# Kernel optimization log

Measured on AMD Instinct MI355X. Metric: run time of the kernel, lower is better.

## Reference

```python
import jax, jax.numpy as jnp
import numpy as np

TEXT_SIZE = 1024
HIDDEN = 512

def setup_inputs() -> dict:
    key = jax.random.key(0)
    k1, k2, k3, k4, k5, k6 = jax.random.split(key, 6)
    B, S, D, H = 32, 4096, TEXT_SIZE, HIDDEN
    text_seq = jax.random.normal(k1, (B, S, D), dtype=jnp.float32)
    previous_hidden = jax.random.normal(k2, (B, D), dtype=jnp.float32)
    # attention_hidden: Linear(D -> H) + ReLU
    W1 = jax.random.normal(k3, (D, H), dtype=jnp.float32) / np.sqrt(D)
    b1 = jax.random.normal(k4, (H,), dtype=jnp.float32) * 0.01
    # attention_scoring: Linear(H -> 1)
    w2 = jax.random.normal(k5, (H,), dtype=jnp.float32) / np.sqrt(H)
    b2 = jax.random.normal(k6, (), dtype=jnp.float32) * 0.01
    return {"text_seq": text_seq, "previous_hidden": previous_hidden,
            "W1": W1, "b1": b1, "w2": w2, "b2": b2}

def reference(text_seq, previous_hidden, W1, b1, w2, b2):
    # text_seq: [B, S, D]; previous_hidden: [B, D]
    # per-timestep: score = Linear1(ReLU(Linear0(prev * h_t))) -> batched here
    prod = text_seq * previous_hidden[:, None, :]          # [B, S, D]
    hidden = jax.nn.relu(jnp.einsum('bsd,dh->bsh', prod, W1) + b1)  # [B, S, H]
    scores = jnp.einsum('bsh,h->bs', hidden, w2) + b2      # [B, S]
    weights = jax.nn.softmax(scores, axis=1)               # [B, S]
    out = jnp.einsum('bsd,bs->bd', text_seq, weights)      # [B, D]
    return out
```

## Files before the change

kernel.cpp:

```cpp
#include <hip/hip_runtime.h>
#include <hip/hip_bf16.h>
#include <stdint.h>

#define B_ 32
#define S_ 4096
#define D_ 1024
#define H_ 512
#define BK 32

typedef __bf16 bf16_t;
typedef bf16_t bf16x8 __attribute__((ext_vector_type(8)));
typedef float f32x4 __attribute__((ext_vector_type(4)));

#define AS_STRIDE 40

__global__ __launch_bounds__(256)
void ta_prep_kernel(const float* __restrict__ W1, bf16_t* __restrict__ W1bf)
{
    const int kb = blockIdx.x;
    const int t  = threadIdx.x;

#pragma unroll
    for (int hh = 0; hh < 2; ++hh) {
        int h = t + hh * 256;
        bf16_t row[BK];
#pragma unroll
        for (int kk = 0; kk < BK; ++kk)
            row[kk] = (bf16_t)W1[(size_t)(kb * BK + kk) * H_ + h];
        bf16_t* dst = W1bf + ((size_t)kb * H_ + h) * BK;
#pragma unroll
        for (int c = 0; c < 4; ++c)
            *(bf16x8*)(dst + c * 8) = *(const bf16x8*)&row[c * 8];
    }
}

__global__ __launch_bounds__(256, 2)
void ta_score_kernel(const float* __restrict__ x,
                     const float* __restrict__ prev,
                     const bf16_t* __restrict__ W1bf,
                     const float* __restrict__ b1,
                     const float* __restrict__ w2,
                     const float* __restrict__ b2,
                     float* __restrict__ scores)
{
    __shared__ bf16_t As[64 * AS_STRIDE];
    __shared__ bf16_t Bs[H_ * BK];
    __shared__ float  scoreS[4][64];

    const int t    = threadIdx.x;
    const int wv   = t >> 6;
    const int lane = t & 63;
    const int quad = lane >> 4;
    const int n16  = lane & 15;

    const int b  = blockIdx.y;
    const int s0 = blockIdx.x * 64;

    const int ar = t >> 2;
    const int ac = (t & 3) * 8;
    const float* xrow  = x + ((size_t)b * S_ + s0 + ar) * D_;
    const float* prevb = prev + (size_t)b * D_;

    float b1v[8], w2v[8];
#pragma unroll
    for (int j = 0; j < 8; ++j) {
        int h = wv * 128 + j * 16 + n16;
        b1v[j] = b1[h];
        w2v[j] = w2[h];
    }

    f32x4 acc[4][8];
#pragma unroll
    for (int i = 0; i < 4; ++i)
#pragma unroll
        for (int j = 0; j < 8; ++j)
            acc[i][j] = (f32x4){0.f, 0.f, 0.f, 0.f};

    for (int kb = 0; kb < D_ / BK; ++kb) {
        f32x4 a0 = *(const f32x4*)(xrow + kb * BK + ac);
        f32x4 a1 = *(const f32x4*)(xrow + kb * BK + ac + 4);
        f32x4 p0 = *(const f32x4*)(prevb + kb * BK + ac);
        f32x4 p1 = *(const f32x4*)(prevb + kb * BK + ac + 4);

        __syncthreads();

        const char* gB = (const char*)(W1bf + (size_t)kb * H_ * BK);
#pragma unroll
        for (int r = 0; r < 8; ++r) {
            int off = (wv * 8 + r) * 1024;
            __builtin_amdgcn_global_load_lds(
                (const __attribute__((address_space(1))) void*)(gB + off + lane * 16),
                (__attribute__((address_space(3))) void*)((char*)Bs + off),
                16, 0, 0);
        }

        {
            a0 *= p0;
            a1 *= p1;
            bf16x8 aw;
#pragma unroll
            for (int e = 0; e < 4; ++e) { aw[e] = (bf16_t)a0[e]; aw[4 + e] = (bf16_t)a1[e]; }
            *(bf16x8*)&As[ar * AS_STRIDE + ac] = aw;
        }

        __syncthreads();

        bf16x8 afr[4];
#pragma unroll
        for (int i = 0; i < 4; ++i)
            afr[i] = *(const bf16x8*)&As[(i * 16 + n16) * AS_STRIDE + quad * 8];
#pragma unroll
        for (int j = 0; j < 8; ++j) {
            bf16x8 bfr = *(const bf16x8*)&Bs[(wv * 128 + j * 16 + n16) * BK + quad * 8];
#pragma unroll
            for (int i = 0; i < 4; ++i)
                acc[i][j] = __builtin_amdgcn_mfma_f32_16x16x32_bf16(afr[i], bfr, acc[i][j], 0, 0, 0);
        }
    }

    float part[4][4];
#pragma unroll
    for (int i = 0; i < 4; ++i)
#pragma unroll
        for (int r = 0; r < 4; ++r) {
            float p = 0.f;
#pragma unroll
            for (int j = 0; j < 8; ++j) {
                float hval = acc[i][j][r] + b1v[j];
                hval = fmaxf(hval, 0.f);
                p += hval * w2v[j];
            }
            for (int off = 8; off > 0; off >>= 1)
                p += __shfl_xor(p, off);
            part[i][r] = p;
        }

    if (n16 == 0) {
#pragma unroll
        for (int i = 0; i < 4; ++i)
#pragma unroll
            for (int r = 0; r < 4; ++r)
                scoreS[wv][i * 16 + quad * 4 + r] = part[i][r];
    }
    __syncthreads();

    if (t < 64) {
        float sc = scoreS[0][t] + scoreS[1][t] + scoreS[2][t] + scoreS[3][t] + b2[0];
        scores[(size_t)b * S_ + s0 + t] = sc;
    }
}

__global__ __launch_bounds__(256)
void ta_softmax_kernel(const float* __restrict__ scores, float* __restrict__ weights)
{
    const int b = blockIdx.x;
    const int t = threadIdx.x;
    const float* s = scores + (size_t)b * S_;

    float v[16];
    float m = -1e30f;
#pragma unroll
    for (int i = 0; i < 16; ++i) {
        v[i] = s[t + i * 256];
        m = fmaxf(m, v[i]);
    }

    __shared__ float red[256];
    red[t] = m;
    __syncthreads();
    for (int off = 128; off > 0; off >>= 1) {
        if (t < off) red[t] = fmaxf(red[t], red[t + off]);
        __syncthreads();
    }
    m = red[0];
    __syncthreads();

    float sum = 0.f;
#pragma unroll
    for (int i = 0; i < 16; ++i) {
        v[i] = __expf(v[i] - m);
        sum += v[i];
    }
    red[t] = sum;
    __syncthreads();
    for (int off = 128; off > 0; off >>= 1) {
        if (t < off) red[t] += red[t + off];
        __syncthreads();
    }
    const float inv = 1.f / red[0];

    float* w = weights + (size_t)b * S_;
#pragma unroll
    for (int i = 0; i < 16; ++i)
        w[t + i * 256] = v[i] * inv;
}

__global__ __launch_bounds__(256)
void ta_wsum_kernel(const float* __restrict__ x, const float* __restrict__ weights,
                    float* __restrict__ out)
{
    const int sc = blockIdx.x;
    const int b  = blockIdx.y;
    const int t  = threadIdx.x;

    __shared__ float wS[128];
    if (t < 128) wS[t] = weights[(size_t)b * S_ + sc * 128 + t];
    __syncthreads();

    const float* xb = x + ((size_t)b * S_ + (size_t)sc * 128) * D_;

    f32x4 acc0 = (f32x4){0.f,0.f,0.f,0.f}, acc1 = acc0, acc2 = acc0, acc3 = acc0;
    for (int s = 0; s < 128; s += 4) {
        f32x4 x0 = *(const f32x4*)(xb + (size_t)(s + 0) * D_ + t * 4);
        f32x4 x1 = *(const f32x4*)(xb + (size_t)(s + 1) * D_ + t * 4);
        f32x4 x2 = *(const f32x4*)(xb + (size_t)(s + 2) * D_ + t * 4);
        f32x4 x3 = *(const f32x4*)(xb + (size_t)(s + 3) * D_ + t * 4);
        acc0 += x0 * wS[s + 0];
        acc1 += x1 * wS[s + 1];
        acc2 += x2 * wS[s + 2];
        acc3 += x3 * wS[s + 3];
    }
    f32x4 r = (acc0 + acc1) + (acc2 + acc3);

    float* o = out + (size_t)b * D_ + t * 4;
    atomicAdd(o + 0, r[0]);
    atomicAdd(o + 1, r[1]);
    atomicAdd(o + 2, r[2]);
    atomicAdd(o + 3, r[3]);
}

extern "C" void kernel_launch(void* const* d_in, const int* in_sizes, int n_in,
                              void* d_out, int out_size, void* d_ws, size_t ws_size,
                              hipStream_t stream) {
    const float* x    = (const float*)d_in[0];
    const float* prev = (const float*)d_in[1];
    const float* W1   = (const float*)d_in[2];
    const float* b1   = (const float*)d_in[3];
    const float* w2   = (const float*)d_in[4];
    const float* b2   = (const float*)d_in[5];
    float* out = (float*)d_out;

    bf16_t* W1bf   = (bf16_t*)d_ws;
    float* scores  = (float*)((char*)d_ws + (size_t)1024 * 1024);
    float* weights = scores + B_ * S_;

    hipMemsetAsync(d_out, 0, (size_t)B_ * D_ * sizeof(float), stream);

    ta_prep_kernel<<<32, 256, 0, stream>>>(W1, W1bf);

    dim3 g1(S_ / 64, B_);
    ta_score_kernel<<<g1, 256, 0, stream>>>(x, prev, W1bf, b1, w2, b2, scores);

    ta_softmax_kernel<<<B_, 256, 0, stream>>>(scores, weights);

    dim3 g3(S_ / 128, B_);
    ta_wsum_kernel<<<g3, 256, 0, stream>>>(x, weights, out);
}
```

Measured before the change: 875.5 us.

## Fuse score, softmax and weighted sum via flash-style chunked online softmax

Folds the softmax and weighted-sum stages into the score kernel. Each 64-row block computes a local max and exp-sum, forms its partial weighted sum of x while that tile is likely still cached, and writes the partial plus (m, l) to workspace. A small combine kernel rescales and sums the 64 partials per batch. This is meant to avoid a second full pass over x from HBM, two kernel launches, the memset and the atomics, at the cost of an 8 MB partial buffer and an extra combine step.

```diff
diff --git a/kernel.cpp b/kernel.cpp
--- a/kernel.cpp
+++ b/kernel.cpp
@@ -7,6 +7,7 @@
 #define D_ 1024
 #define H_ 512
 #define BK 32
+#define NCHUNK 64
 
 typedef __bf16 bf16_t;
 typedef bf16_t bf16x8 __attribute__((ext_vector_type(8)));
@@ -35,17 +36,19 @@
 }
 
 __global__ __launch_bounds__(256, 2)
-void ta_score_kernel(const float* __restrict__ x,
+void ta_fused_kernel(const float* __restrict__ x,
                      const float* __restrict__ prev,
                      const bf16_t* __restrict__ W1bf,
                      const float* __restrict__ b1,
                      const float* __restrict__ w2,
                      const float* __restrict__ b2,
-                     float* __restrict__ scores)
+                     float* __restrict__ pout,
+                     float* __restrict__ mlbuf)
 {
     __shared__ bf16_t As[64 * AS_STRIDE];
     __shared__ bf16_t Bs[H_ * BK];
     __shared__ float  scoreS[4][64];
+    __shared__ float  wS[64];
 
     const int t    = threadIdx.x;
     const int wv   = t >> 6;
@@ -146,71 +149,27 @@
 
     if (t < 64) {
         float sc = scoreS[0][t] + scoreS[1][t] + scoreS[2][t] + scoreS[3][t] + b2[0];
-        scores[(size_t)b * S_ + s0 + t] = sc;
-    }
-}
-
-__global__ __launch_bounds__(256)
-void ta_softmax_kernel(const float* __restrict__ scores, float* __restrict__ weights)
-{
-    const int b = blockIdx.x;
-    const int t = threadIdx.x;
-    const float* s = scores + (size_t)b * S_;
-
-    float v[16];
-    float m = -1e30f;
-#pragma unroll
-    for (int i = 0; i < 16; ++i) {
-        v[i] = s[t + i * 256];
-        m = fmaxf(m, v[i]);
-    }
-
-    __shared__ float red[256];
-    red[t] = m;
+        float m = sc;
+#pragma unroll
+        for (int off = 32; off > 0; off >>= 1)
+            m = fmaxf(m, __shfl_xor(m, off));
+        float wexp = __expf(sc - m);
+        float l = wexp;
+#pragma unroll
+        for (int off = 32; off > 0; off >>= 1)
+            l += __shfl_xor(l, off);
+        wS[t] = wexp;
+        if (t == 0) {
+            float* ml = mlbuf + ((size_t)b * NCHUNK + blockIdx.x) * 2;
+            ml[0] = m;
+            ml[1] = l;
+        }
+    }
     __syncthreads();
-    for (int off = 128; off > 0; off >>= 1) {
-        if (t < off) red[t] = fmaxf(red[t], red[t + off]);
-        __syncthreads();
-    }
-    m = red[0];
-    __syncthreads();
-
-    float sum = 0.f;
-#pragma unroll
-    for (int i = 0; i < 16; ++i) {
-        v[i] = __expf(v[i] - m);
-        sum += v[i];
-    }
-    red[t] = sum;
-    __syncthreads();
-    for (int off = 128; off > 0; off >>= 1) {
-        if (t < off) red[t] += red[t + off];
-        __syncthreads();
-    }
-    const float inv = 1.f / red[0];
-
-    float* w = weights + (size_t)b * S_;
-#pragma unroll
-    for (int i = 0; i < 16; ++i)
-        w[t + i * 256] = v[i] * inv;
-}
-
-__global__ __launch_bounds__(256)
-void ta_wsum_kernel(const float* __restrict__ x, const float* __restrict__ weights,
-                    float* __restrict__ out)
-{
-    const int sc = blockIdx.x;
-    const int b  = blockIdx.y;
-    const int t  = threadIdx.x;
-
-    __shared__ float wS[128];
-    if (t < 128) wS[t] = weights[(size_t)b * S_ + sc * 128 + t];
-    __syncthreads();
-
-    const float* xb = x + ((size_t)b * S_ + (size_t)sc * 128) * D_;
-
+
+    const float* xb = x + ((size_t)b * S_ + s0) * D_;
     f32x4 acc0 = (f32x4){0.f,0.f,0.f,0.f}, acc1 = acc0, acc2 = acc0, acc3 = acc0;
-    for (int s = 0; s < 128; s += 4) {
+    for (int s = 0; s < 64; s += 4) {
         f32x4 x0 = *(const f32x4*)(xb + (size_t)(s + 0) * D_ + t * 4);
         f32x4 x1 = *(const f32x4*)(xb + (size_t)(s + 1) * D_ + t * 4);
         f32x4 x2 = *(const f32x4*)(xb + (size_t)(s + 2) * D_ + t * 4);
@@ -221,12 +180,46 @@
         acc3 += x3 * wS[s + 3];
     }
     f32x4 r = (acc0 + acc1) + (acc2 + acc3);
-
-    float* o = out + (size_t)b * D_ + t * 4;
-    atomicAdd(o + 0, r[0]);
-    atomicAdd(o + 1, r[1]);
-    atomicAdd(o + 2, r[2]);
-    atomicAdd(o + 3, r[3]);
+    *(f32x4*)(pout + ((size_t)b * NCHUNK + blockIdx.x) * D_ + t * 4) = r;
+}
+
+__global__ __launch_bounds__(256)
+void ta_combine_kernel(const float* __restrict__ pout,
+                       const float* __restrict__ mlbuf,
+                       float* __restrict__ out)
+{
+    const int b = blockIdx.y;
+    const int t = threadIdx.x;
+    const int d = blockIdx.x * 256 + t;
+
+    __shared__ float scaleS[NCHUNK];
+    if (t < NCHUNK) {
+        const float* ml = mlbuf + ((size_t)b * NCHUNK + t) * 2;
+        float m = ml[0];
+        float l = ml[1];
+        float M = m;
+#pragma unroll
+        for (int off = 32; off > 0; off >>= 1)
+            M = fmaxf(M, __shfl_xor(M, off));
+        float le = l * __expf(m - M);
+        float L = le;
+#pragma unroll
+        for (int off = 32; off > 0; off >>= 1)
+            L += __shfl_xor(L, off);
+        scaleS[t] = __expf(m - M) / L;
+    }
+    __syncthreads();
+
+    const float* pb = pout + (size_t)b * NCHUNK * D_ + d;
+    float a0 = 0.f, a1 = 0.f, a2 = 0.f, a3 = 0.f;
+#pragma unroll 4
+    for (int c = 0; c < NCHUNK; c += 4) {
+        a0 += pb[(size_t)(c + 0) * D_] * scaleS[c + 0];
+        a1 += pb[(size_t)(c + 1) * D_] * scaleS[c + 1];
+        a2 += pb[(size_t)(c + 2) * D_] * scaleS[c + 2];
+        a3 += pb[(size_t)(c + 3) * D_] * scaleS[c + 3];
+    }
+    out[(size_t)b * D_ + d] = (a0 + a1) + (a2 + a3);
 }
 
 extern "C" void kernel_launch(void* const* d_in, const int* in_sizes, int n_in,
@@ -240,19 +233,15 @@
     const float* b2   = (const float*)d_in[5];
     float* out = (float*)d_out;
 
-    bf16_t* W1bf   = (bf16_t*)d_ws;
-    float* scores  = (float*)((char*)d_ws + (size_t)1024 * 1024);
-    float* weights = scores + B_ * S_;
-
-    hipMemsetAsync(d_out, 0, (size_t)B_ * D_ * sizeof(float), stream);
+    bf16_t* W1bf  = (bf16_t*)d_ws;
+    float*  pout  = (float*)((char*)d_ws + (size_t)1 * 1024 * 1024);
+    float*  mlbuf = (float*)((char*)d_ws + (size_t)9 * 1024 * 1024);
 
     ta_prep_kernel<<<32, 256, 0, stream>>>(W1, W1bf);
 
-    dim3 g1(S_ / 64, B_);
-    ta_score_kernel<<<g1, 256, 0, stream>>>(x, prev, W1bf, b1, w2, b2, scores);
-
-    ta_softmax_kernel<<<B_, 256, 0, stream>>>(scores, weights);
-
-    dim3 g3(S_ / 128, B_);
-    ta_wsum_kernel<<<g3, 256, 0, stream>>>(x, weights, out);
-}
+    dim3 g1(NCHUNK, B_);
+    ta_fused_kernel<<<g1, 256, 0, stream>>>(x, prev, W1bf, b1, w2, b2, pout, mlbuf);
+
+    dim3 g2(D_ / 256, B_);
+    ta_combine_kernel<<<g2, 256, 0, stream>>>(pout, mlbuf, out);
+}
```

Measured after the change: 838.8 us. 4.2% less time.
